# Kernel optimization log

Measured on AMD Instinct MI355X. Metric: run time of the kernel, lower is better.

## Reference

```python
import jax, jax.numpy as jnp
import numpy as np
from jax.scipy.special import i0

IM_SIZE = (256, 256)
GRID_SIZE = (512, 512)
NUMPOINTS = 6
OS = GRID_SIZE[0] / IM_SIZE[0]
# Beatty et al. optimal Kaiser-Bessel shape parameter
BETA = float(np.pi * np.sqrt((NUMPOINTS / OS) ** 2 * (OS - 0.5) ** 2 - 0.8))


def _apod_1d(N, G):
    # 1/FT(kb kernel) scaling coefficients (de-apodization), static numpy
    x = np.arange(N) - N / 2.0
    arg = np.pi * NUMPOINTS * x / G
    t = BETA ** 2 - arg ** 2  # > 0 for this config
    ph = np.sinh(np.sqrt(t)) / np.sqrt(t)
    return (1.0 / ph).astype(np.float32)


def _kb(u):
    # Kaiser-Bessel interpolation kernel, support |u| <= NUMPOINTS/2
    x = 2.0 * u / NUMPOINTS
    t = 1.0 - x * x
    inside = t > 0
    t = jnp.where(inside, t, 0.0)
    return jnp.where(inside, i0(BETA * jnp.sqrt(t)), 0.0)


def setup_inputs():
    key = jax.random.key(0)
    k1, k2, k3 = jax.random.split(key, 3)
    B, M = 8, 131072
    image = jax.random.normal(k1, (B,) + IM_SIZE, dtype=jnp.float32)
    ktraj = (jax.random.uniform(k2, (B, 2, M), dtype=jnp.float32) * 2.0 - 1.0) * jnp.pi
    dcf = jax.random.uniform(k3, (B, M), dtype=jnp.float32)
    return {"image": image, "ktraj": ktraj, "dcf": dcf}


def _nufft(image, ktraj, dcf):
    B = image.shape[0]
    N1, N2 = IM_SIZE
    G1, G2 = GRID_SIZE
    J = NUMPOINTS
    # 1) de-apodization (scaling coefficients), separable per-dim
    a1 = jnp.asarray(_apod_1d(N1, G1))
    a2 = jnp.asarray(_apod_1d(N2, G2))
    img = image.astype(jnp.complex64) * (a1[:, None] * a2[None, :])
    # 2) centered zero-pad to oversampled grid, FFT with DC at bin 0
    p1, p2 = (G1 - N1) // 2, (G2 - N2) // 2
    grid = jnp.zeros((B, G1, G2), dtype=jnp.complex64).at[:, p1:p1 + N1, p2:p2 + N2].set(img)
    kgrid = jnp.fft.fft2(jnp.fft.ifftshift(grid, axes=(1, 2)))
    # 3) KB interpolation (gather) at non-uniform points
    tm1 = ktraj[:, 0] * (G1 / (2.0 * jnp.pi))  # (B,M) in grid units
    tm2 = ktraj[:, 1] * (G2 / (2.0 * jnp.pi))
    offs = jnp.arange(J, dtype=jnp.float32) - (J // 2 - 1)  # [-2..3]
    g1 = jnp.floor(tm1)[..., None] + offs  # (B,M,J) neighbor coords
    g2 = jnp.floor(tm2)[..., None] + offs
    w1 = _kb(tm1[..., None] - g1)
    w2 = _kb(tm2[..., None] - g2)
    i1 = jnp.mod(g1.astype(jnp.int32), G1)
    i2 = jnp.mod(g2.astype(jnp.int32), G2)
    lin = (i1[..., :, None] * G2 + i2[..., None, :]).reshape(B, -1)  # (B, M*J*J)
    vals = jnp.take_along_axis(kgrid.reshape(B, -1), lin, axis=1).reshape(B, -1, J, J)
    w = (w1[..., :, None] * w2[..., None, :]).astype(jnp.complex64)
    kdata = jnp.sum(vals * w, axis=(-1, -2))  # (B,M) complex
    kdata = kdata * dcf
    return jnp.stack([kdata.real, kdata.imag], axis=0)  # (2,B,M) float32


def reference(image, ktraj, dcf):
    return _nufft(image, ktraj, dcf)
```

## Files before the change

kernel.cpp:

```cpp
#include <hip/hip_runtime.h>
#include <math.h>

#define GSZ 512
#define NSZ 256
#define NBATCH 8
#define MPTS 131072
#define PI_F 3.14159265358979f
#define BETA_F 13.8551004f
#define BETA2_F (BETA_F * BETA_F)
#define RSQ2 0.70710678f
#define PADIDX(i) ((i) + ((i) >> 3))


__device__ __forceinline__ float apod(int i) {
    float x = (float)(i - 128);
    float arg = PI_F * 6.0f * x * (1.0f / 512.0f);
    float t = BETA2_F - arg * arg;
    float st = sqrtf(t);
    return st / sinhf(st);
}

__device__ __forceinline__ float bessi0(float x) {
    float ax = fabsf(x);
    if (ax < 3.75f) {
        float y = ax * (1.0f / 3.75f);
        y *= y;
        return 1.0f + y * (3.5156229f + y * (3.0899424f + y * (1.2067492f
             + y * (0.2659732f + y * (0.0360768f + y * 0.0045813f)))));
    } else {
        float y = 3.75f / ax;
        float p = 0.39894228f + y * (0.01328592f + y * (0.00225319f + y * (-0.00157565f
             + y * (0.00916281f + y * (-0.02057706f + y * (0.02635537f + y * (-0.01647633f
             + y * 0.00392377f)))))));
        return p * __expf(ax) * rsqrtf(ax);
    }
}

__device__ __forceinline__ float kbweight(float u) {
    float x = u * (1.0f / 3.0f);
    float t = 1.0f - x * x;
    return (t > 0.f) ? bessi0(BETA_F * sqrtf(t)) : 0.f;
}

__device__ __forceinline__ float2 cadd(float2 a, float2 b){ return make_float2(a.x+b.x, a.y+b.y); }
__device__ __forceinline__ float2 csub(float2 a, float2 b){ return make_float2(a.x-b.x, a.y-b.y); }
__device__ __forceinline__ float2 cmul(float2 a, float2 b){ return make_float2(a.x*b.x-a.y*b.y, a.x*b.y+a.y*b.x); }
__device__ __forceinline__ float2 mul_negi(float2 a){ return make_float2(a.y, -a.x); }
__device__ __forceinline__ float2 mul_posi(float2 a){ return make_float2(-a.y, a.x); }
__device__ __forceinline__ float2 mul_w81(float2 a){ return make_float2(RSQ2*(a.x+a.y), RSQ2*(a.y-a.x)); }
__device__ __forceinline__ float2 mul_w83(float2 a){ return make_float2(RSQ2*(a.y-a.x), -RSQ2*(a.x+a.y)); }

__device__ __forceinline__ void dft8_combine(float2 E0, float2 E1, float2 E2, float2 E3,
                                             float2 O0, float2 O1, float2 O2, float2 O3,
                                             float2* y) {
    float2 c1 = mul_w81(O1), c2 = mul_negi(O2), c3 = mul_w83(O3);
    y[0] = cadd(E0, O0); y[4] = csub(E0, O0);
    y[1] = cadd(E1, c1); y[5] = csub(E1, c1);
    y[2] = cadd(E2, c2); y[6] = csub(E2, c2);
    y[3] = cadd(E3, c3); y[7] = csub(E3, c3);
}

__device__ __forceinline__ void dft8(const float2* x, float2* y) {
    float2 a0=x[0], a1=x[2], a2=x[4], a3=x[6];
    float2 b0=x[1], b1=x[3], b2=x[5], b3=x[7];
    float2 ta0=cadd(a0,a2), ta1=csub(a0,a2), ta2=cadd(a1,a3), ta3=csub(a1,a3);
    float2 E0=cadd(ta0,ta2), E2=csub(ta0,ta2);
    float2 E1=cadd(ta1, mul_negi(ta3)), E3=cadd(ta1, mul_posi(ta3));
    float2 tb0=cadd(b0,b2), tb1=csub(b0,b2), tb2=cadd(b1,b3), tb3=csub(b1,b3);
    float2 O0=cadd(tb0,tb2), O2=csub(tb0,tb2);
    float2 O1=cadd(tb1, mul_negi(tb3)), O3=cadd(tb1, mul_posi(tb3));
    dft8_combine(E0,E1,E2,E3,O0,O1,O2,O3,y);
}

__device__ __forceinline__ void dft8_pruned(float2 x0, float2 x1, float2 x6, float2 x7, float2* y) {
    float2 E0 = cadd(x0, x6), E2 = csub(x0, x6);
    float2 E1 = cadd(x0, mul_posi(x6)), E3 = cadd(x0, mul_negi(x6));
    float2 O0 = cadd(x1, x7), O2 = csub(x1, x7);
    float2 O1 = cadd(x1, mul_posi(x7)), O3 = cadd(x1, mul_negi(x7));
    dft8_combine(E0,E1,E2,E3,O0,O1,O2,O3,y);
}

template<int S>
__device__ __forceinline__ void twiddle8(int t, float2* y) {
    if (S < 2) {
        int j = (S == 0) ? t : (t >> 3);
        const float scale = (S == 0) ? (-2.0f*PI_F/512.0f) : (-2.0f*PI_F/64.0f);
        float theta = scale * (float)j;
        float sn, cs;
        __sincosf(theta, &sn, &cs);
        float2 w = make_float2(cs, sn), wq = w;
        y[1] = cmul(y[1], wq);
        #pragma unroll
        for (int q = 2; q < 8; ++q) { wq = cmul(wq, w); y[q] = cmul(y[q], wq); }
    }
}

__global__ __launch_bounds__(256) void pass1_rowfft(const float* __restrict__ image,
                                                    float2* __restrict__ T) {
    __shared__ float2 sm[2][4][578];
    int tid = threadIdx.x;
    int r = tid >> 6, t = tid & 63;
    int blk = blockIdx.x;
    int b = blk & 7;
    int g = blk >> 3;
    int y0 = (g < 32) ? (g << 2) : ((g << 2) + 256);
    int y = y0 + r;
    int iy = (y < 128) ? (y + 128) : (y - 384);
    float ay = apod(iy);
    const float* irow = image + ((size_t)(b * NSZ + iy)) * NSZ;

    float2 y8[8];
    {
        int ix0 = t + 128, ix1 = t + 192, ix6 = t, ix7 = t + 64;
        float2 x0 = make_float2(irow[ix0] * ay * apod(ix0), 0.f);
        float2 x1 = make_float2(irow[ix1] * ay * apod(ix1), 0.f);
        float2 x6 = make_float2(irow[ix6] * ay * apod(ix6), 0.f);
        float2 x7 = make_float2(irow[ix7] * ay * apod(ix7), 0.f);
        dft8_pruned(x0, x1, x6, x7, y8);
        twiddle8<0>(t, y8);
    }
    float2* A  = sm[0][r];
    float2* Bf = sm[1][r];
    #pragma unroll
    for (int q = 0; q < 8; ++q) A[PADIDX((t << 3) + q)] = y8[q];
    __syncthreads();
    {
        float2 x[8];
        #pragma unroll
        for (int p = 0; p < 8; ++p) x[p] = A[PADIDX(t + (p << 6))];
        dft8(x, y8);
        twiddle8<1>(t, y8);
        int j = t >> 3, k = t & 7, base = k + (j << 6);
        #pragma unroll
        for (int q = 0; q < 8; ++q) Bf[PADIDX(base + (q << 3))] = y8[q];
    }
    __syncthreads();
    {
        float2 x[8];
        #pragma unroll
        for (int p = 0; p < 8; ++p) x[p] = Bf[PADIDX(t + (p << 6))];
        dft8(x, y8);
        float2* Trow = T + (((size_t)(b << 9) + y) << 9);
        #pragma unroll
        for (int q = 0; q < 8; ++q) Trow[t + (q << 6)] = y8[q];
    }
}

__global__ __launch_bounds__(256) void pass2_colfft(const float2* __restrict__ T,
                                                    float2* __restrict__ kgrid) {
    __shared__ float2 sm[2][4][578];
    int tid = threadIdx.x;
    int blk = blockIdx.x;
    int b = blk & 7;
    int colbase = (blk >> 3) << 2;
    const float2* Tb = T + ((size_t)b << 18);
    float2* Kb = kgrid + ((size_t)b << 18);

    {
        int c = tid & 3, rr = tid >> 2;
        #pragma unroll
        for (int ei = 0; ei < 4; ++ei) {
            int e = (ei < 2) ? ei : (ei + 4);
            int row = rr + (e << 6);
            sm[0][c][PADIDX(row)] = Tb[((size_t)row << 9) + colbase + c];
        }
    }
    __syncthreads();
    int col = tid >> 6, t = tid & 63;
    float2* A  = sm[0][col];
    float2* Bf = sm[1][col];
    float2 y8[8];
    {
        float2 x0 = A[PADIDX(t)];
        float2 x1 = A[PADIDX(t + 64)];
        float2 x6 = A[PADIDX(t + 384)];
        float2 x7 = A[PADIDX(t + 448)];
        dft8_pruned(x0, x1, x6, x7, y8);
        twiddle8<0>(t, y8);
    }
    #pragma unroll
    for (int q = 0; q < 8; ++q) Bf[PADIDX((t << 3) + q)] = y8[q];
    __syncthreads();
    {
        float2 x[8];
        #pragma unroll
        for (int p = 0; p < 8; ++p) x[p] = Bf[PADIDX(t + (p << 6))];
        dft8(x, y8);
        twiddle8<1>(t, y8);
        int j = t >> 3, k = t & 7, base = k + (j << 6);
        #pragma unroll
        for (int q = 0; q < 8; ++q) A[PADIDX(base + (q << 3))] = y8[q];
    }
    __syncthreads();
    {
        float2 x[8];
        #pragma unroll
        for (int p = 0; p < 8; ++p) x[p] = A[PADIDX(t + (p << 6))];
        dft8(x, y8);
        #pragma unroll
        for (int q = 0; q < 8; ++q) Bf[PADIDX(t + (q << 6))] = y8[q];
    }
    __syncthreads();
    {
        int c = tid & 3, rr = tid >> 2;
        #pragma unroll
        for (int e = 0; e < 8; ++e) {
            int row = rr + (e << 6);
            Kb[((size_t)row << 9) + colbase + c] = sm[1][c][PADIDX(row)];
        }
    }
}

__global__ __launch_bounds__(256) void interp_kb(const float* __restrict__ ktraj,
                                                 const float* __restrict__ dcf,
                                                 const float2* __restrict__ kgrid,
                                                 float* __restrict__ out) {
    int tid = threadIdx.x;
    int blk = blockIdx.x;
    int b = blk & 7;
    int g = tid >> 3;
    int j = tid & 7;
    int m = ((blk >> 3) << 5) + g;
    int gid = (b << 17) + m;

    const float SCALE = (float)GSZ / (2.0f * PI_F);
    float tm1 = ktraj[((size_t)b * 2) * MPTS + m] * SCALE;
    float tm2 = ktraj[((size_t)b * 2 + 1) * MPTS + m] * SCALE;
    float f1 = floorf(tm1), f2 = floorf(tm2);
    int if1 = (int)f1, if2 = (int)f2;

    float w2_own = kbweight(tm2 - f2 - (float)(j - 2));
    int   i2_own = (if2 + j - 2) & 511;
    float w1_own = kbweight(tm1 - f1 - (float)(j - 2));

    int lane = tid & 63;
    int gbase = lane & 56;

    const float2* Kb = kgrid + ((size_t)b << 18);
    float s_re = 0.f, s_im = 0.f;
    #pragma unroll
    for (int a = 0; a < 6; ++a) {
        int i1a = (if1 + a - 2) & 511;
        float w1a = __shfl(w1_own, gbase + a, 64);
        float2 v = Kb[((size_t)i1a << 9) + i2_own];
        s_re = fmaf(w1a, v.x, s_re);
        s_im = fmaf(w1a, v.y, s_im);
    }
    float p_re = w2_own * s_re;
    float p_im = w2_own * s_im;
    #pragma unroll
    for (int d = 1; d < 8; d <<= 1) {
        p_re += __shfl_xor(p_re, d, 64);
        p_im += __shfl_xor(p_im, d, 64);
    }
    float dd = dcf[gid];
    if (j == 0) out[gid] = p_re * dd;
    if (j == 1) out[gid + NBATCH * MPTS] = p_im * dd;
}


extern "C" void kernel_launch(void* const* d_in, const int* in_sizes, int n_in,
                              void* d_out, int out_size, void* d_ws, size_t ws_size,
                              hipStream_t stream) {
    const float* image = (const float*)d_in[0];
    const float* ktraj = (const float*)d_in[1];
    const float* dcf   = (const float*)d_in[2];
    float* out = (float*)d_out;

    float2* T     = (float2*)d_ws;
    float2* kgrid = T + (size_t)NBATCH * GSZ * GSZ;

    pass1_rowfft<<<NBATCH * 64, 256, 0, stream>>>(image, T);
    pass2_colfft<<<NBATCH * 128, 256, 0, stream>>>(T, kgrid);
    interp_kb<<<NBATCH * (MPTS / 32), 256, 0, stream>>>(ktraj, dcf, kgrid, out);
}
```

Before: 132.1 us.

## Compact row-FFT buffer, batch 8 columns per block, use KB weight LUT

Pass 1 now writes only the 256 non-zero rows into a compact intermediate buffer, halving its size and write traffic. Pass 2 processes 8 columns per block with two FFTs per thread and reads only the compact rows. The interpolation kernel replaces per-weight Bessel evaluation with a shared-memory lookup table in squared distance with linear interpolation, and each block now handles 512 points. The table adds a small approximation error and per-block setup work, and fewer larger blocks may reduce latency hiding.

```diff
diff --git a/kernel.cpp b/kernel.cpp
--- a/kernel.cpp
+++ b/kernel.cpp
@@ -10,6 +10,7 @@
 #define BETA2_F (BETA_F * BETA_F)
 #define RSQ2 0.70710678f
 #define PADIDX(i) ((i) + ((i) >> 3))
+#define LUTN 768
 
 
 __device__ __forceinline__ float apod(int i) {
@@ -36,10 +37,14 @@
     }
 }
 
-__device__ __forceinline__ float kbweight(float u) {
-    float x = u * (1.0f / 3.0f);
-    float t = 1.0f - x * x;
-    return (t > 0.f) ? bessi0(BETA_F * sqrtf(t)) : 0.f;
+__device__ __forceinline__ float kblut(const float* __restrict__ lut, float u) {
+    float s = u * u;
+    float p = s * ((float)LUTN / 9.0f);
+    p = fminf(p, (float)(LUTN - 1));
+    int i = (int)p;
+    float f = p - (float)i;
+    float w = fmaf(f, lut[i + 1] - lut[i], lut[i]);
+    return (s < 9.0f) ? w : 0.f;
 }
 
 __device__ __forceinline__ float2 cadd(float2 a, float2 b){ return make_float2(a.x+b.x, a.y+b.y); }
@@ -103,8 +108,8 @@
     int blk = blockIdx.x;
     int b = blk & 7;
     int g = blk >> 3;
-    int y0 = (g < 32) ? (g << 2) : ((g << 2) + 256);
-    int y = y0 + r;
+    int rp = (g << 2) + r;
+    int y = (rp < 128) ? rp : (rp + 256);
     int iy = (y < 128) ? (y + 128) : (y - 384);
     float ay = apod(iy);
     const float* irow = image + ((size_t)(b * NSZ + iy)) * NSZ;
@@ -140,7 +145,7 @@
         #pragma unroll
         for (int p = 0; p < 8; ++p) x[p] = Bf[PADIDX(t + (p << 6))];
         dft8(x, y8);
-        float2* Trow = T + (((size_t)(b << 9) + y) << 9);
+        float2* Trow = T + (((size_t)(b << 8) + rp) << 9);
         #pragma unroll
         for (int q = 0; q < 8; ++q) Trow[t + (q << 6)] = y8[q];
     }
@@ -148,65 +153,80 @@
 
 __global__ __launch_bounds__(256) void pass2_colfft(const float2* __restrict__ T,
                                                     float2* __restrict__ kgrid) {
-    __shared__ float2 sm[2][4][578];
+    __shared__ float2 B[8][578];
     int tid = threadIdx.x;
     int blk = blockIdx.x;
     int b = blk & 7;
-    int colbase = (blk >> 3) << 2;
-    const float2* Tb = T + ((size_t)b << 18);
+    int colbase = (blk >> 3) << 3;
+    const float2* Tb = T + ((size_t)b << 17);
     float2* Kb = kgrid + ((size_t)b << 18);
 
     {
-        int c = tid & 3, rr = tid >> 2;
-        #pragma unroll
-        for (int ei = 0; ei < 4; ++ei) {
-            int e = (ei < 2) ? ei : (ei + 4);
-            int row = rr + (e << 6);
-            sm[0][c][PADIDX(row)] = Tb[((size_t)row << 9) + colbase + c];
-        }
-    }
-    __syncthreads();
-    int col = tid >> 6, t = tid & 63;
-    float2* A  = sm[0][col];
-    float2* Bf = sm[1][col];
-    float2 y8[8];
-    {
-        float2 x0 = A[PADIDX(t)];
-        float2 x1 = A[PADIDX(t + 64)];
-        float2 x6 = A[PADIDX(t + 384)];
-        float2 x7 = A[PADIDX(t + 448)];
-        dft8_pruned(x0, x1, x6, x7, y8);
-        twiddle8<0>(t, y8);
-    }
+        int c = tid & 7, r0 = tid >> 3;
+        #pragma unroll
+        for (int k = 0; k < 8; ++k) {
+            int rr = r0 + (k << 5);
+            B[c][PADIDX(rr)] = Tb[((size_t)rr << 9) + colbase + c];
+        }
+    }
+    __syncthreads();
+    int t = tid & 63;
+    int c0 = tid >> 6;
+    float2 ya[8], yb[8];
+    {
+        float2* Ba = B[c0];
+        float2* Bb = B[c0 + 4];
+        float2 a0 = Ba[PADIDX(t)],   a1 = Ba[PADIDX(t + 64)];
+        float2 a6 = Ba[PADIDX(t + 128)], a7 = Ba[PADIDX(t + 192)];
+        float2 b0 = Bb[PADIDX(t)],   b1 = Bb[PADIDX(t + 64)];
+        float2 b6 = Bb[PADIDX(t + 128)], b7 = Bb[PADIDX(t + 192)];
+        dft8_pruned(a0, a1, a6, a7, ya); twiddle8<0>(t, ya);
+        dft8_pruned(b0, b1, b6, b7, yb); twiddle8<0>(t, yb);
+    }
+    __syncthreads();
     #pragma unroll
-    for (int q = 0; q < 8; ++q) Bf[PADIDX((t << 3) + q)] = y8[q];
-    __syncthreads();
-    {
-        float2 x[8];
-        #pragma unroll
-        for (int p = 0; p < 8; ++p) x[p] = Bf[PADIDX(t + (p << 6))];
-        dft8(x, y8);
-        twiddle8<1>(t, y8);
+    for (int q = 0; q < 8; ++q) {
+        B[c0][PADIDX((t << 3) + q)]     = ya[q];
+        B[c0 + 4][PADIDX((t << 3) + q)] = yb[q];
+    }
+    __syncthreads();
+    {
+        float2 xa[8], xb[8];
+        #pragma unroll
+        for (int p = 0; p < 8; ++p) { xa[p] = B[c0][PADIDX(t + (p << 6))]; xb[p] = B[c0 + 4][PADIDX(t + (p << 6))]; }
+        dft8(xa, ya); twiddle8<1>(t, ya);
+        dft8(xb, yb); twiddle8<1>(t, yb);
+    }
+    __syncthreads();
+    {
         int j = t >> 3, k = t & 7, base = k + (j << 6);
         #pragma unroll
-        for (int q = 0; q < 8; ++q) A[PADIDX(base + (q << 3))] = y8[q];
-    }
-    __syncthreads();
-    {
-        float2 x[8];
-        #pragma unroll
-        for (int p = 0; p < 8; ++p) x[p] = A[PADIDX(t + (p << 6))];
-        dft8(x, y8);
-        #pragma unroll
-        for (int q = 0; q < 8; ++q) Bf[PADIDX(t + (q << 6))] = y8[q];
-    }
-    __syncthreads();
-    {
-        int c = tid & 3, rr = tid >> 2;
-        #pragma unroll
-        for (int e = 0; e < 8; ++e) {
-            int row = rr + (e << 6);
-            Kb[((size_t)row << 9) + colbase + c] = sm[1][c][PADIDX(row)];
+        for (int q = 0; q < 8; ++q) {
+            B[c0][PADIDX(base + (q << 3))]     = ya[q];
+            B[c0 + 4][PADIDX(base + (q << 3))] = yb[q];
+        }
+    }
+    __syncthreads();
+    {
+        float2 xa[8], xb[8];
+        #pragma unroll
+        for (int p = 0; p < 8; ++p) { xa[p] = B[c0][PADIDX(t + (p << 6))]; xb[p] = B[c0 + 4][PADIDX(t + (p << 6))]; }
+        dft8(xa, ya);
+        dft8(xb, yb);
+    }
+    __syncthreads();
+    #pragma unroll
+    for (int q = 0; q < 8; ++q) {
+        B[c0][PADIDX(t + (q << 6))]     = ya[q];
+        B[c0 + 4][PADIDX(t + (q << 6))] = yb[q];
+    }
+    __syncthreads();
+    {
+        int c = tid & 7, r0 = tid >> 3;
+        #pragma unroll
+        for (int k = 0; k < 16; ++k) {
+            int rr = r0 + (k << 5);
+            Kb[((size_t)rr << 9) + colbase + c] = B[c][PADIDX(rr)];
         }
     }
 }
@@ -215,47 +235,64 @@
                                                  const float* __restrict__ dcf,
                                                  const float2* __restrict__ kgrid,
                                                  float* __restrict__ out) {
+    __shared__ float lut[LUTN + 1];
     int tid = threadIdx.x;
+    for (int i = tid; i <= LUTN; i += 256) {
+        float s = (float)i * (9.0f / (float)LUTN);
+        float tt = fmaxf(1.0f - s * (1.0f / 9.0f), 0.f);
+        lut[i] = bessi0(BETA_F * sqrtf(tt));
+    }
+    __syncthreads();
+
     int blk = blockIdx.x;
     int b = blk & 7;
-    int g = tid >> 3;
+    int gb = blk >> 3;
     int j = tid & 7;
-    int m = ((blk >> 3) << 5) + g;
-    int gid = (b << 17) + m;
-
-    const float SCALE = (float)GSZ / (2.0f * PI_F);
-    float tm1 = ktraj[((size_t)b * 2) * MPTS + m] * SCALE;
-    float tm2 = ktraj[((size_t)b * 2 + 1) * MPTS + m] * SCALE;
-    float f1 = floorf(tm1), f2 = floorf(tm2);
-    int if1 = (int)f1, if2 = (int)f2;
-
-    float w2_own = kbweight(tm2 - f2 - (float)(j - 2));
-    int   i2_own = (if2 + j - 2) & 511;
-    float w1_own = kbweight(tm1 - f1 - (float)(j - 2));
-
+    int gloc = tid >> 3;
     int lane = tid & 63;
     int gbase = lane & 56;
 
+    const float SCALE = (float)GSZ / (2.0f * PI_F);
     const float2* Kb = kgrid + ((size_t)b << 18);
-    float s_re = 0.f, s_im = 0.f;
-    #pragma unroll
-    for (int a = 0; a < 6; ++a) {
-        int i1a = (if1 + a - 2) & 511;
-        float w1a = __shfl(w1_own, gbase + a, 64);
-        float2 v = Kb[((size_t)i1a << 9) + i2_own];
-        s_re = fmaf(w1a, v.x, s_re);
-        s_im = fmaf(w1a, v.y, s_im);
-    }
-    float p_re = w2_own * s_re;
-    float p_im = w2_own * s_im;
-    #pragma unroll
-    for (int d = 1; d < 8; d <<= 1) {
-        p_re += __shfl_xor(p_re, d, 64);
-        p_im += __shfl_xor(p_im, d, 64);
-    }
-    float dd = dcf[gid];
-    if (j == 0) out[gid] = p_re * dd;
-    if (j == 1) out[gid + NBATCH * MPTS] = p_im * dd;
+    const float* kt1 = ktraj + ((size_t)(b * 2)) * MPTS;
+    const float* kt2 = kt1 + MPTS;
+    const float* dcfb = dcf + ((size_t)b << 17);
+    float* out_re = out + ((size_t)b << 17);
+    float* out_im = out_re + (size_t)NBATCH * MPTS;
+
+    int m0 = (gb << 9) + gloc;
+    #pragma unroll 2
+    for (int it = 0; it < 16; ++it) {
+        int m = m0 + (it << 5);
+        float tm1 = kt1[m] * SCALE;
+        float tm2 = kt2[m] * SCALE;
+        float f1 = floorf(tm1), f2 = floorf(tm2);
+        int if1 = (int)f1, if2 = (int)f2;
+
+        float w2_own = kblut(lut, tm2 - f2 - (float)(j - 2));
+        int   i2_own = (if2 + j - 2) & 511;
+        float w1_own = kblut(lut, tm1 - f1 - (float)(j - 2));
+
+        float s_re = 0.f, s_im = 0.f;
+        #pragma unroll
+        for (int a = 0; a < 6; ++a) {
+            int i1a = (if1 + a - 2) & 511;
+            float w1a = __shfl(w1_own, gbase + a, 64);
+            float2 v = Kb[((size_t)i1a << 9) + i2_own];
+            s_re = fmaf(w1a, v.x, s_re);
+            s_im = fmaf(w1a, v.y, s_im);
+        }
+        float p_re = w2_own * s_re;
+        float p_im = w2_own * s_im;
+        #pragma unroll
+        for (int d = 1; d < 8; d <<= 1) {
+            p_re += __shfl_xor(p_re, d, 64);
+            p_im += __shfl_xor(p_im, d, 64);
+        }
+        float dd = dcfb[m];
+        if (j == 0) out_re[m] = p_re * dd;
+        if (j == 1) out_im[m] = p_im * dd;
+    }
 }
 
 
@@ -268,9 +305,9 @@
     float* out = (float*)d_out;
 
     float2* T     = (float2*)d_ws;
-    float2* kgrid = T + (size_t)NBATCH * GSZ * GSZ;
+    float2* kgrid = T + (size_t)NBATCH * 256 * GSZ;
 
     pass1_rowfft<<<NBATCH * 64, 256, 0, stream>>>(image, T);
-    pass2_colfft<<<NBATCH * 128, 256, 0, stream>>>(T, kgrid);
-    interp_kb<<<NBATCH * (MPTS / 32), 256, 0, stream>>>(ktraj, dcf, kgrid, out);
-}
+    pass2_colfft<<<NBATCH * 64, 256, 0, stream>>>(T, kgrid);
+    interp_kb<<<NBATCH * 256, 256, 0, stream>>>(ktraj, dcf, kgrid, out);
+}
```

New measurement: 133.1 us. About the same (+0.8%).

## Approximate KB weight asymptotically, compact row-FFT buffer, single-wave FFT blocks, persistent interp loop

Applied to the files above, without the earlier changes.

Swaps the piecewise polynomial Bessel I0 for a single asymptotic expansion (exp(x)/sqrt(2πx) times a short series in 1/x), with the argument clamped at small x. This removes a divergent branch and many FMAs from the interpolation weights, but the expansion is inaccurate where the argument is small, near the edges of the kernel support. The row and column FFTs now run as one 64-thread wavefront per block with no __syncthreads, and the intermediate buffer keeps only the 256 nonzero rows, so the workspace is half the size. The interpolation kernel loops over 16 point groups per block to amortize setup and reduce the block count.

```diff
diff --git a/kernel.cpp b/kernel.cpp
--- a/kernel.cpp
+++ b/kernel.cpp
@@ -20,26 +20,14 @@
     return st / sinhf(st);
 }
 
-__device__ __forceinline__ float bessi0(float x) {
-    float ax = fabsf(x);
-    if (ax < 3.75f) {
-        float y = ax * (1.0f / 3.75f);
-        y *= y;
-        return 1.0f + y * (3.5156229f + y * (3.0899424f + y * (1.2067492f
-             + y * (0.2659732f + y * (0.0360768f + y * 0.0045813f)))));
-    } else {
-        float y = 3.75f / ax;
-        float p = 0.39894228f + y * (0.01328592f + y * (0.00225319f + y * (-0.00157565f
-             + y * (0.00916281f + y * (-0.02057706f + y * (0.02635537f + y * (-0.01647633f
-             + y * 0.00392377f)))))));
-        return p * __expf(ax) * rsqrtf(ax);
-    }
-}
-
-__device__ __forceinline__ float kbweight(float u) {
-    float x = u * (1.0f / 3.0f);
-    float t = 1.0f - x * x;
-    return (t > 0.f) ? bessi0(BETA_F * sqrtf(t)) : 0.f;
+__device__ __forceinline__ float kbw(float u) {
+    float t = 1.0f - u * u * (1.0f / 9.0f);
+    float x = BETA_F * sqrtf(fmaxf(t, 0.0f));
+    float xc = fmaxf(x, 0.35f);
+    float r = __builtin_amdgcn_rcpf(xc);
+    float poly = 1.0f + r * (0.125f + r * 0.0703125f);
+    float w = __expf(xc) * __builtin_amdgcn_rsqf(6.2831853f * xc) * poly;
+    return (t > 0.0f) ? w : 0.0f;
 }
 
 __device__ __forceinline__ float2 cadd(float2 a, float2 b){ return make_float2(a.x+b.x, a.y+b.y); }
@@ -95,16 +83,14 @@
     }
 }
 
-__global__ __launch_bounds__(256) void pass1_rowfft(const float* __restrict__ image,
-                                                    float2* __restrict__ T) {
-    __shared__ float2 sm[2][4][578];
-    int tid = threadIdx.x;
-    int r = tid >> 6, t = tid & 63;
+__global__ __launch_bounds__(64) void pass1_rowfft(const float* __restrict__ image,
+                                                   float2* __restrict__ T) {
+    __shared__ float2 A[578];
+    int t = threadIdx.x;
     int blk = blockIdx.x;
     int b = blk & 7;
-    int g = blk >> 3;
-    int y0 = (g < 32) ? (g << 2) : ((g << 2) + 256);
-    int y = y0 + r;
+    int rp = blk >> 3;
+    int y = (rp < 128) ? rp : (rp + 256);
     int iy = (y < 128) ? (y + 128) : (y - 384);
     float ay = apod(iy);
     const float* irow = image + ((size_t)(b * NSZ + iy)) * NSZ;
@@ -119,11 +105,8 @@
         dft8_pruned(x0, x1, x6, x7, y8);
         twiddle8<0>(t, y8);
     }
-    float2* A  = sm[0][r];
-    float2* Bf = sm[1][r];
     #pragma unroll
     for (int q = 0; q < 8; ++q) A[PADIDX((t << 3) + q)] = y8[q];
-    __syncthreads();
     {
         float2 x[8];
         #pragma unroll
@@ -132,81 +115,76 @@
         twiddle8<1>(t, y8);
         int j = t >> 3, k = t & 7, base = k + (j << 6);
         #pragma unroll
-        for (int q = 0; q < 8; ++q) Bf[PADIDX(base + (q << 3))] = y8[q];
-    }
-    __syncthreads();
+        for (int q = 0; q < 8; ++q) A[PADIDX(base + (q << 3))] = y8[q];
+    }
     {
         float2 x[8];
         #pragma unroll
-        for (int p = 0; p < 8; ++p) x[p] = Bf[PADIDX(t + (p << 6))];
+        for (int p = 0; p < 8; ++p) x[p] = A[PADIDX(t + (p << 6))];
         dft8(x, y8);
-        float2* Trow = T + (((size_t)(b << 9) + y) << 9);
+        float2* Trow = T + (((size_t)(b << 8) + rp) << 9);
         #pragma unroll
         for (int q = 0; q < 8; ++q) Trow[t + (q << 6)] = y8[q];
     }
 }
 
-__global__ __launch_bounds__(256) void pass2_colfft(const float2* __restrict__ T,
-                                                    float2* __restrict__ kgrid) {
-    __shared__ float2 sm[2][4][578];
-    int tid = threadIdx.x;
+__global__ __launch_bounds__(64) void pass2_colfft(const float2* __restrict__ T,
+                                                   float2* __restrict__ kgrid) {
+    __shared__ float2 B[4][578];
+    int t = threadIdx.x;
     int blk = blockIdx.x;
     int b = blk & 7;
     int colbase = (blk >> 3) << 2;
-    const float2* Tb = T + ((size_t)b << 18);
+    const float2* Tb = T + ((size_t)b << 17);
     float2* Kb = kgrid + ((size_t)b << 18);
 
     {
-        int c = tid & 3, rr = tid >> 2;
-        #pragma unroll
-        for (int ei = 0; ei < 4; ++ei) {
-            int e = (ei < 2) ? ei : (ei + 4);
-            int row = rr + (e << 6);
-            sm[0][c][PADIDX(row)] = Tb[((size_t)row << 9) + colbase + c];
-        }
-    }
-    __syncthreads();
-    int col = tid >> 6, t = tid & 63;
-    float2* A  = sm[0][col];
-    float2* Bf = sm[1][col];
-    float2 y8[8];
-    {
-        float2 x0 = A[PADIDX(t)];
-        float2 x1 = A[PADIDX(t + 64)];
-        float2 x6 = A[PADIDX(t + 384)];
-        float2 x7 = A[PADIDX(t + 448)];
-        dft8_pruned(x0, x1, x6, x7, y8);
-        twiddle8<0>(t, y8);
+        int c = t & 3, r0 = t >> 2;
+        #pragma unroll
+        for (int k = 0; k < 16; ++k) {
+            int rr = r0 + (k << 4);
+            B[c][PADIDX(rr)] = Tb[((size_t)rr << 9) + colbase + c];
+        }
     }
     #pragma unroll
-    for (int q = 0; q < 8; ++q) Bf[PADIDX((t << 3) + q)] = y8[q];
-    __syncthreads();
-    {
-        float2 x[8];
-        #pragma unroll
-        for (int p = 0; p < 8; ++p) x[p] = Bf[PADIDX(t + (p << 6))];
-        dft8(x, y8);
-        twiddle8<1>(t, y8);
-        int j = t >> 3, k = t & 7, base = k + (j << 6);
-        #pragma unroll
-        for (int q = 0; q < 8; ++q) A[PADIDX(base + (q << 3))] = y8[q];
-    }
-    __syncthreads();
-    {
-        float2 x[8];
-        #pragma unroll
-        for (int p = 0; p < 8; ++p) x[p] = A[PADIDX(t + (p << 6))];
-        dft8(x, y8);
-        #pragma unroll
-        for (int q = 0; q < 8; ++q) Bf[PADIDX(t + (q << 6))] = y8[q];
-    }
-    __syncthreads();
-    {
-        int c = tid & 3, rr = tid >> 2;
-        #pragma unroll
-        for (int e = 0; e < 8; ++e) {
-            int row = rr + (e << 6);
-            Kb[((size_t)row << 9) + colbase + c] = sm[1][c][PADIDX(row)];
+    for (int c = 0; c < 4; ++c) {
+        float2* Bc = B[c];
+        float2 y8[8];
+        {
+            float2 x0 = Bc[PADIDX(t)];
+            float2 x1 = Bc[PADIDX(t + 64)];
+            float2 x6 = Bc[PADIDX(t + 128)];
+            float2 x7 = Bc[PADIDX(t + 192)];
+            dft8_pruned(x0, x1, x6, x7, y8);
+            twiddle8<0>(t, y8);
+            #pragma unroll
+            for (int q = 0; q < 8; ++q) Bc[PADIDX((t << 3) + q)] = y8[q];
+        }
+        {
+            float2 x[8];
+            #pragma unroll
+            for (int p = 0; p < 8; ++p) x[p] = Bc[PADIDX(t + (p << 6))];
+            dft8(x, y8);
+            twiddle8<1>(t, y8);
+            int j = t >> 3, k = t & 7, base = k + (j << 6);
+            #pragma unroll
+            for (int q = 0; q < 8; ++q) Bc[PADIDX(base + (q << 3))] = y8[q];
+        }
+        {
+            float2 x[8];
+            #pragma unroll
+            for (int p = 0; p < 8; ++p) x[p] = Bc[PADIDX(t + (p << 6))];
+            dft8(x, y8);
+            #pragma unroll
+            for (int q = 0; q < 8; ++q) Bc[PADIDX(t + (q << 6))] = y8[q];
+        }
+    }
+    {
+        int c = t & 3, r0 = t >> 2;
+        #pragma unroll
+        for (int k = 0; k < 32; ++k) {
+            int rr = r0 + (k << 4);
+            Kb[((size_t)rr << 9) + colbase + c] = B[c][PADIDX(rr)];
         }
     }
 }
@@ -218,44 +196,53 @@
     int tid = threadIdx.x;
     int blk = blockIdx.x;
     int b = blk & 7;
-    int g = tid >> 3;
+    int gb = blk >> 3;
     int j = tid & 7;
-    int m = ((blk >> 3) << 5) + g;
-    int gid = (b << 17) + m;
-
-    const float SCALE = (float)GSZ / (2.0f * PI_F);
-    float tm1 = ktraj[((size_t)b * 2) * MPTS + m] * SCALE;
-    float tm2 = ktraj[((size_t)b * 2 + 1) * MPTS + m] * SCALE;
-    float f1 = floorf(tm1), f2 = floorf(tm2);
-    int if1 = (int)f1, if2 = (int)f2;
-
-    float w2_own = kbweight(tm2 - f2 - (float)(j - 2));
-    int   i2_own = (if2 + j - 2) & 511;
-    float w1_own = kbweight(tm1 - f1 - (float)(j - 2));
-
+    int gloc = tid >> 3;
     int lane = tid & 63;
     int gbase = lane & 56;
 
+    const float SCALE = (float)GSZ / (2.0f * PI_F);
     const float2* Kb = kgrid + ((size_t)b << 18);
-    float s_re = 0.f, s_im = 0.f;
-    #pragma unroll
-    for (int a = 0; a < 6; ++a) {
-        int i1a = (if1 + a - 2) & 511;
-        float w1a = __shfl(w1_own, gbase + a, 64);
-        float2 v = Kb[((size_t)i1a << 9) + i2_own];
-        s_re = fmaf(w1a, v.x, s_re);
-        s_im = fmaf(w1a, v.y, s_im);
-    }
-    float p_re = w2_own * s_re;
-    float p_im = w2_own * s_im;
-    #pragma unroll
-    for (int d = 1; d < 8; d <<= 1) {
-        p_re += __shfl_xor(p_re, d, 64);
-        p_im += __shfl_xor(p_im, d, 64);
-    }
-    float dd = dcf[gid];
-    if (j == 0) out[gid] = p_re * dd;
-    if (j == 1) out[gid + NBATCH * MPTS] = p_im * dd;
+    const float* kt1 = ktraj + ((size_t)(b * 2)) * MPTS;
+    const float* kt2 = kt1 + MPTS;
+    const float* dcfb = dcf + ((size_t)b << 17);
+    float* out_re = out + ((size_t)b << 17);
+    float* out_im = out_re + (size_t)NBATCH * MPTS;
+
+    int m0 = (gb << 9) + gloc;
+    #pragma unroll 2
+    for (int it = 0; it < 16; ++it) {
+        int m = m0 + (it << 5);
+        float tm1 = kt1[m] * SCALE;
+        float tm2 = kt2[m] * SCALE;
+        float f1 = floorf(tm1), f2 = floorf(tm2);
+        int if1 = (int)f1, if2 = (int)f2;
+
+        float w2_own = kbw(tm2 - f2 - (float)(j - 2));
+        int   i2_own = (if2 + j - 2) & 511;
+        float w1_own = kbw(tm1 - f1 - (float)(j - 2));
+
+        float s_re = 0.f, s_im = 0.f;
+        #pragma unroll
+        for (int a = 0; a < 6; ++a) {
+            int i1a = (if1 + a - 2) & 511;
+            float w1a = __shfl(w1_own, gbase + a, 64);
+            float2 v = Kb[((size_t)i1a << 9) + i2_own];
+            s_re = fmaf(w1a, v.x, s_re);
+            s_im = fmaf(w1a, v.y, s_im);
+        }
+        float p_re = w2_own * s_re;
+        float p_im = w2_own * s_im;
+        #pragma unroll
+        for (int d = 1; d < 8; d <<= 1) {
+            p_re += __shfl_xor(p_re, d, 64);
+            p_im += __shfl_xor(p_im, d, 64);
+        }
+        float dd = dcfb[m];
+        if (j == 0) out_re[m] = p_re * dd;
+        if (j == 1) out_im[m] = p_im * dd;
+    }
 }
 
 
@@ -268,9 +255,9 @@
     float* out = (float*)d_out;
 
     float2* T     = (float2*)d_ws;
-    float2* kgrid = T + (size_t)NBATCH * GSZ * GSZ;
-
-    pass1_rowfft<<<NBATCH * 64, 256, 0, stream>>>(image, T);
-    pass2_colfft<<<NBATCH * 128, 256, 0, stream>>>(T, kgrid);
-    interp_kb<<<NBATCH * (MPTS / 32), 256, 0, stream>>>(ktraj, dcf, kgrid, out);
-}
+    float2* kgrid = T + (size_t)NBATCH * 256 * GSZ;
+
+    pass1_rowfft<<<NBATCH * 256, 64, 0, stream>>>(image, T);
+    pass2_colfft<<<NBATCH * 128, 64, 0, stream>>>(T, kgrid);
+    interp_kb<<<NBATCH * 256, 256, 0, stream>>>(ktraj, dcf, kgrid, out);
+}
```

Result: slower. 135.1 us (+2.3%).
